# Kernel tuning notes

Hardware: AMD Instinct MI355X
Metric: run time of the kernel (lower is better)

Reference implementation:

```python
import jax, jax.numpy as jnp
import numpy as np
import math

B, N, G, D = 32, 100, 32, 1024  # batch, boxes (hardcoded 100), groups/fc_dim, out_channel
DG = D // G                      # 32, per-group dim
FEAT_DIM = 64                    # position embedding dim


def setup_inputs() -> dict:
    key = jax.random.key(0)
    ks = jax.random.split(key, 10)
    feat = jax.random.normal(ks[0], (B, N, D), dtype=jnp.float32)
    # valid boxes: xmin/ymin in [0,500), width/height in [1,101)
    xy = jax.random.uniform(ks[1], (B, N, 2), dtype=jnp.float32) * 500.0
    wh = jax.random.uniform(ks[2], (B, N, 2), dtype=jnp.float32) * 100.0 + 1.0
    bbox = jnp.concatenate([xy, xy + wh], axis=-1)  # (B,N,4) xmin,ymin,xmax,ymax
    feat_mask = jax.random.bernoulli(ks[3], 0.1, (B, N, G, N))
    s = 0.02
    fc1_w = jax.random.normal(ks[4], (G, FEAT_DIM), dtype=jnp.float32) * s
    fc1_b = jnp.zeros((G,), dtype=jnp.float32)
    q_w = jax.random.normal(ks[5], (D, D), dtype=jnp.float32) * s
    q_b = jnp.zeros((D,), dtype=jnp.float32)
    k_w = jax.random.normal(ks[6], (D, D), dtype=jnp.float32) * s
    k_b = jnp.zeros((D,), dtype=jnp.float32)
    # grouped 1x1 conv: torch weight (D_out=1024, D_in/groups=1024,1,1) -> (G, DG, D)
    conv_w = jax.random.normal(ks[7], (G, DG, D), dtype=jnp.float32) * s
    conv_b = jnp.zeros((D,), dtype=jnp.float32)
    return {"feat": feat, "bbox": bbox, "feat_mask": feat_mask,
            "fc1_w": fc1_w, "fc1_b": fc1_b, "q_w": q_w, "q_b": q_b,
            "k_w": k_w, "k_b": k_b, "conv_w": conv_w, "conv_b": conv_b}


def _position_embedding(bbox):
    xmin, ymin, xmax, ymax = jnp.split(bbox, 4, axis=2)  # each (B,N,1)
    bw = xmax - xmin + 1.0
    bh = ymax - ymin + 1.0
    cx = 0.5 * (xmin + xmax)
    cy = 0.5 * (ymin + ymax)
    dx = jnp.log(jnp.maximum(jnp.abs((cx - cx.swapaxes(1, 2)) / bw), 1e-3))
    dy = jnp.log(jnp.maximum(jnp.abs((cy - cy.swapaxes(1, 2)) / bh), 1e-3))
    dw = jnp.log(bw / bw.swapaxes(1, 2))
    dh = jnp.log(bh / bh.swapaxes(1, 2))
    pos = jnp.stack([dx, dy, dw, dh], axis=3)  # (B,N,N,4)
    feat_range = jnp.arange(FEAT_DIM // 8, dtype=jnp.float32)  # 8
    dim_mat = jnp.power(1000.0, (8.0 / FEAT_DIM) * feat_range)  # (8,)
    div = (100.0 * pos)[..., None] / dim_mat  # (B,N,N,4,8)
    emb = jnp.concatenate([jnp.sin(div), jnp.cos(div)], axis=4)  # (B,N,N,4,16)
    return emb.reshape(bbox.shape[0], N, N, FEAT_DIM)


def reference(feat, bbox, feat_mask, fc1_w, fc1_b, q_w, q_b, k_w, k_b, conv_w, conv_b):
    pos_emb = _position_embedding(bbox)  # (B,N,N,64)
    # fc1 + relu -> affinity weights; aff_weight[b,q,g,k]
    aff_weight = jax.nn.relu(jnp.einsum('bqkf,gf->bqkg', pos_emb, fc1_w) + fc1_b)
    aff_weight = aff_weight.swapaxes(2, 3)  # (B,N,G,N)
    q = (feat @ q_w.T + q_b).reshape(-1, N, G, DG)  # (B,N,G,DG)
    k = (feat @ k_w.T + k_b).reshape(-1, N, G, DG)
    aff = jnp.einsum('bqgd,bkgd->bqgk', q, k) * (1.0 / math.sqrt(DG))  # (B,N,G,N)
    weighted = jnp.log(jnp.maximum(aff_weight, 1e-6)) + aff
    weighted = jnp.where(feat_mask, -1e9, weighted)
    sm = jax.nn.softmax(weighted, axis=3)  # (B,N,G,N)
    out_t = jnp.einsum('bqgk,bkc->bqgc', sm, feat)  # (B,N,G,D)
    # grouped 1x1 conv: group g maps D channels -> DG output channels
    lin = jnp.einsum('bqgc,goc->bqgo', out_t, conv_w) + conv_b.reshape(G, DG)
    attention = lin.reshape(feat.shape[0], N, D)
    return jax.nn.relu(feat + attention)
```

## Files before the change

kernel.cpp:

```cpp
#include <hip/hip_runtime.h>
#include <math.h>

#define B_  32
#define N_  100
#define G_  32
#define D_  1024
#define DG_ 32
#define FD_ 64

typedef __attribute__((ext_vector_type(8))) short short8;
typedef __attribute__((ext_vector_type(8))) unsigned short ushort8;
typedef __attribute__((ext_vector_type(4))) unsigned short ushort4v;
typedef __attribute__((ext_vector_type(4))) float f32x4;

__device__ inline unsigned short f2bf(float f) {
    unsigned int x = __float_as_uint(f);
    unsigned int r = (x + 0x7fffu + ((x >> 16) & 1u)) >> 16;
    return (unsigned short)r;
}
__device__ inline unsigned short f2h(float f) {
    _Float16 h = (_Float16)f;
    return __builtin_bit_cast(unsigned short, h);
}
__device__ inline float h2f(unsigned short u) {
    return (float)__builtin_bit_cast(_Float16, u);
}
__device__ inline void load_lds16(const void* g, void* l) {
    __builtin_amdgcn_global_load_lds(
        (const __attribute__((address_space(1))) void*)g,
        (__attribute__((address_space(3))) void*)l, 16, 0, 0);
}

__global__ __launch_bounds__(256) void prep_kernel(
    const unsigned int* __restrict__ mask, int* __restrict__ flag,
    const float* __restrict__ bbox, float* __restrict__ prep,
    const float* __restrict__ feat, unsigned short* __restrict__ featb,
    const float* __restrict__ qw, unsigned short* __restrict__ wqb,
    const float* __restrict__ kw, unsigned short* __restrict__ wkb,
    const float* __restrict__ cw, unsigned short* __restrict__ wcb)
{
    const int bid = blockIdx.x;
    const int t = threadIdx.x;
    if (bid < 256) {
        const int nwords = (B_ * N_ * G_ * N_) / 4 / 8;
        int v = 0;
        for (int i = bid * 256 + t; i < nwords; i += 256 * 256)
            v |= (mask[i] > 1u) ? 1 : 0;
        if (__any(v) && (t & 63) == 0) atomicOr(flag, 1);
        return;
    }
    if (bid < 272) {
        const int i = (bid - 256) * 256 + t;
        if (i < B_ * N_) {
            const float4 bb = *reinterpret_cast<const float4*>(bbox + (size_t)i * 4);
            const float bw = bb.z - bb.x + 1.0f, bh = bb.w - bb.y + 1.0f;
            float4 o0, o1;
            o0.x = 0.5f * (bb.x + bb.z);
            o0.y = 0.5f * (bb.y + bb.w);
            o0.z = __logf(bw);
            o0.w = __logf(bh);
            o1.x = 1.0f / bw;
            o1.y = 1.0f / bh;
            o1.z = 0.0f; o1.w = 0.0f;
            *reinterpret_cast<float4*>(prep + (size_t)i * 8)     = o0;
            *reinterpret_cast<float4*>(prep + (size_t)i * 8 + 4) = o1;
        }
        return;
    }
    const float* src;
    unsigned short* dst;
    int i;
    if (bid < 1872)      { src = feat; dst = featb; i = (bid - 272) * 256 + t; }
    else if (bid < 2384) { src = qw;   dst = wqb;   i = (bid - 1872) * 256 + t; }
    else if (bid < 2896) { src = kw;   dst = wkb;   i = (bid - 2384) * 256 + t; }
    else                 { src = cw;   dst = wcb;   i = (bid - 2896) * 256 + t; }
    const float4 a = reinterpret_cast<const float4*>(src)[i * 2 + 0];
    const float4 b = reinterpret_cast<const float4*>(src)[i * 2 + 1];
    ushort8 o;
    o[0] = f2bf(a.x); o[1] = f2bf(a.y); o[2] = f2bf(a.z); o[3] = f2bf(a.w);
    o[4] = f2bf(b.x); o[5] = f2bf(b.y); o[6] = f2bf(b.z); o[7] = f2bf(b.w);
    *reinterpret_cast<ushort8*>(&dst[i * 8]) = o;
}

__global__ __launch_bounds__(256) void mfma_gemm_nt(
    const unsigned short* __restrict__ A,
    const unsigned short* __restrict__ Wq,
    const unsigned short* __restrict__ Wk,
    const unsigned short* __restrict__ Wc,
    const float* __restrict__ bq, const float* __restrict__ bk,
    unsigned short* __restrict__ Q16, unsigned short* __restrict__ K16,
    unsigned short* __restrict__ F16)
{
    __shared__ short As0[128 * 64], As1[128 * 64];
    __shared__ short Bs0[64 * 64],  Bs1[64 * 64];

    const int z = blockIdx.z;
    const unsigned short* W = (z == 0) ? Wq : (z == 1) ? Wk : Wc;
    const float* bias        = (z == 0) ? bq : (z == 1) ? bk : nullptr;
    unsigned short* O        = (z == 0) ? Q16 : (z == 1) ? K16 : F16;

    const int m0 = blockIdx.x * 128;
    const int n0 = blockIdx.y * 64;
    const int t = threadIdx.x;
    const int lane = t & 63;
    const int wid = t >> 6;
    const int wr = wid >> 1, wc = wid & 1;
    const int lo = lane & 15, hi = lane >> 4;

    f32x4 acc[4][2] = {};

    auto STAGE = [&](short* dA, short* dB, int k0) {
#pragma unroll
        for (int c = 0; c < 4; ++c) {
            const int idx16 = c * 256 + t;
            const int row = idx16 >> 3;
            const int colb = ((idx16 & 7) * 16) ^ ((row & 7) << 4);
            load_lds16((const char*)(A + (size_t)(m0 + row) * D_ + k0) + colb,
                       (char*)dA + (c * 256 + wid * 64) * 16);
        }
#pragma unroll
        for (int c = 0; c < 2; ++c) {
            const int idx16 = c * 256 + t;
            const int row = idx16 >> 3;
            const int colb = ((idx16 & 7) * 16) ^ ((row & 7) << 4);
            load_lds16((const char*)(W + (size_t)(n0 + row) * D_ + k0) + colb,
                       (char*)dB + (c * 256 + wid * 64) * 16);
        }
    };

    auto COMPUTE = [&](const short* sA, const short* sB) {
#pragma unroll
        for (int ks = 0; ks < 2; ++ks) {
            short8 afr[4], bfr[2];
            const int kb = ks * 64 + hi * 16;
#pragma unroll
            for (int f = 0; f < 4; ++f) {
                const int am = wr * 64 + f * 16 + lo;
                afr[f] = *reinterpret_cast<const short8*>(
                    (const char*)sA + am * 128 + (kb ^ ((am & 7) << 4)));
            }
#pragma unroll
            for (int j = 0; j < 2; ++j) {
                const int bn = wc * 32 + j * 16 + lo;
                bfr[j] = *reinterpret_cast<const short8*>(
                    (const char*)sB + bn * 128 + (kb ^ ((bn & 7) << 4)));
            }
#pragma unroll
            for (int i = 0; i < 4; ++i)
#pragma unroll
                for (int j = 0; j < 2; ++j)
                    acc[i][j] = __builtin_amdgcn_mfma_f32_16x16x32_bf16(
                        afr[i], bfr[j], acc[i][j], 0, 0, 0);
        }
    };

    STAGE(As0, Bs0, 0);
    __syncthreads();
    for (int it = 0; it < 16; it += 2) {
        STAGE(As1, Bs1, (it + 1) << 6);
        COMPUTE(As0, Bs0);
        __syncthreads();
        if (it + 2 < 16) STAGE(As0, Bs0, (it + 2) << 6);
        COMPUTE(As1, Bs1);
        __syncthreads();
    }

#pragma unroll
    for (int j = 0; j < 2; ++j) {
        const int col = n0 + wc * 32 + j * 16 + lo;
        const float bv = bias ? bias[col] : 0.0f;
#pragma unroll
        for (int i = 0; i < 4; ++i) {
            const int mbase = m0 + wr * 64 + i * 16 + hi * 4;
#pragma unroll
            for (int r = 0; r < 4; ++r)
                O[(size_t)(mbase + r) * D_ + col] = f2bf(acc[i][j][r] + bv);
        }
    }
}

__global__ __launch_bounds__(256) void pos_fc1_kernel(
    const float* __restrict__ prep, const float* __restrict__ fc1_w,
    const float* __restrict__ fc1_b,
    const unsigned char* __restrict__ mask8, const int* __restrict__ mask32,
    const int* __restrict__ flag, unsigned short* __restrict__ wm)
{
    __shared__ unsigned short embh[112 * 72];
    __shared__ unsigned short w1h[G_ * 72];
    __shared__ float b1[G_];
    __shared__ float tbl[8];
    __shared__ float pos4[N_][4];

    const int b = blockIdx.x / N_;
    const int q = blockIdx.x % N_;
    const int t = threadIdx.x;
    const int lane = t & 63;
    const int w = t >> 6;
    const int lo = lane & 15, hi = lane >> 4;

    const float4 pq0 = *reinterpret_cast<const float4*>(prep + (size_t)(b * N_ + q) * 8);
    const float4 pq1 = *reinterpret_cast<const float4*>(prep + (size_t)(b * N_ + q) * 8 + 4);
    const float cxq = pq0.x, cyq = pq0.y, lbwq = pq0.z, lbhq = pq0.w;
    const float rbwq = pq1.x, rbhq = pq1.y;

    for (int i = t; i < G_ * FD_; i += 256)
        w1h[(i >> 6) * 72 + (i & 63)] = f2h(fc1_w[i]);
    if (t < G_) b1[t] = fc1_b[t];
    if (t < 8)  tbl[t] = 100.0f / powf(1000.0f, (float)t * 0.125f);
    for (int i = t; i < 12 * 64; i += 256)
        embh[(100 + (i >> 6)) * 72 + (i & 63)] = 0;

    if (t < N_) {
        const float4 p0 = *reinterpret_cast<const float4*>(prep + (size_t)(b * N_ + t) * 8);
        pos4[t][0] = __logf(fmaxf(fabsf(cxq - p0.x) * rbwq, 1e-3f));
        pos4[t][1] = __logf(fmaxf(fabsf(cyq - p0.y) * rbhq, 1e-3f));
        pos4[t][2] = lbwq - p0.z;
        pos4[t][3] = lbhq - p0.w;
    }
    __syncthreads();

    for (int idx = t; idx < N_ * 32; idx += 256) {
        const int k = idx >> 5;
        const int p = (idx >> 3) & 3;
        const int j = idx & 7;
        const float dv = pos4[k][p] * tbl[j];
        embh[k * 72 + p * 16 + j]     = f2h(__sinf(dv));
        embh[k * 72 + p * 16 + 8 + j] = f2h(__cosf(dv));
    }
    __syncthreads();

    const bool bytemask = (*flag != 0);
    const int xq = q & 7;
    for (int tid = w; tid < 14; tid += 4) {
        const int mt = tid >> 1, nt = tid & 1;
        f32x4 d = {};
#pragma unroll
        for (int ks = 0; ks < 2; ++ks) {
            const short8 af = *reinterpret_cast<const short8*>(
                embh + (mt * 16 + lo) * 72 + ks * 32 + hi * 8);
            const short8 bf = *reinterpret_cast<const short8*>(
                w1h + (nt * 16 + lo) * 72 + ks * 32 + hi * 8);
            d = __builtin_amdgcn_mfma_f32_16x16x32_f16(af, bf, d, 0, 0, 0);
        }
        const int g = nt * 16 + lo;
        const int k0 = mt * 16 + hi * 4;
        const float bb = b1[g];
        unsigned int mby = 0;
        uint4 mi = {};
        if (k0 < N_) {
            const size_t midx = ((size_t)(b * N_ + q) * G_ + g) * N_ + k0;
            if (bytemask) mby = *(const unsigned int*)(mask8 + midx);
            else          mi  = *(const uint4*)(mask32 + midx);
        }
        ushort4v ov;
#pragma unroll
        for (int r = 0; r < 4; ++r) {
            const int k = k0 + r;
            const bool msk = bytemask
                ? (((mby >> (8 * r)) & 0xffu) != 0u)
                : ((r == 0 ? mi.x : r == 1 ? mi.y : r == 2 ? mi.z : mi.w) != 0u);
            const float aff = d[r] + bb;
            const float lv = __logf(fmaxf(fmaxf(aff, 0.0f), 1e-6f));
            ov[r] = f2h((k >= N_ || msk) ? -65504.0f : lv);
        }
        const size_t row = (size_t)(b * N_ + q) * G_ + g;
        char* dst = (char*)wm + row * 256 + ((2 * k0) ^ (xq << 4));
        *reinterpret_cast<ushort4v*>(dst) = ov;
    }
}

__global__ __launch_bounds__(256) void attn_mfma(
    const unsigned short* __restrict__ qb, const unsigned short* __restrict__ kb,
    const unsigned short* __restrict__ fk16, const unsigned short* __restrict__ wm,
    const float* __restrict__ feat, const float* __restrict__ conv_b,
    float* __restrict__ out)
{
    __shared__ unsigned short PW[128 * 128];
    __shared__ unsigned short FL[DG_ * 128];

    const int bg = blockIdx.x;
    const int b = bg >> 5, g = bg & 31;
    const int t = threadIdx.x;
    const int lane = t & 63;
    const int w = t >> 6;
    const int lo = lane & 15, hi = lane >> 4;
    const float scale = 0.17677669529663687f;

    {
        const char* wbase = (const char*)wm + ((size_t)b * N_ * G_ + g) * 256;
        for (int u = t; u < 1600; u += 256) {
            const int qq = u >> 4, seg = u & 15;
            load_lds16(wbase + (size_t)qq * (G_ * 256) + seg * 16,
                       (char*)PW + u * 16);
        }
    }
    for (int u = t; u < DG_ * 28; u += 256) {
        const int dg = u / 28, n = 100 + u % 28;
        *(unsigned short*)((char*)FL + dg * 256 +
                           (((n >> 3) ^ (dg & 7)) << 4) + (n & 7) * 2) = 0;
    }
    for (int u = t; u < 400; u += 256) {
        const int n = u >> 2, c4 = u & 3;
        const ushort8 v = *reinterpret_cast<const ushort8*>(
            fk16 + (size_t)(b * N_ + n) * D_ + g * DG_ + c4 * 8);
#pragma unroll
        for (int j = 0; j < 8; ++j) {
            const int dg = c4 * 8 + j;
            *(unsigned short*)((char*)FL + dg * 256 +
                               (((n >> 3) ^ j) << 4) + (n & 7) * 2) = v[j];
        }
    }

    short8 qf[2], kf[7];
#pragma unroll
    for (int mtl = 0; mtl < 2; ++mtl) {
        const int row = w * 32 + mtl * 16 + lo;
        const int rc = row < N_ ? row : N_ - 1;
        qf[mtl] = *reinterpret_cast<const short8*>(
            qb + (size_t)(b * N_ + rc) * D_ + g * DG_ + hi * 8);
    }
#pragma unroll
    for (int ct = 0; ct < 7; ++ct) {
        const int kr = ct * 16 + lo;
        const int krc = kr < N_ ? kr : N_ - 1;
        kf[ct] = *reinterpret_cast<const short8*>(
            kb + (size_t)(b * N_ + krc) * D_ + g * DG_ + hi * 8);
    }

    __syncthreads();

    f32x4 s[2][7];
#pragma unroll
    for (int mtl = 0; mtl < 2; ++mtl)
#pragma unroll
        for (int ct = 0; ct < 7; ++ct) {
            f32x4 z = {};
            s[mtl][ct] = __builtin_amdgcn_mfma_f32_16x16x32_bf16(
                qf[mtl], kf[ct], z, 0, 0, 0);
        }

#pragma unroll
    for (int mtl = 0; mtl < 2; ++mtl) {
        const int qr0 = w * 32 + mtl * 16 + hi * 4;
#pragma unroll
        for (int ct = 0; ct < 7; ++ct) {
            const int k = ct * 16 + lo;
#pragma unroll
            for (int r = 0; r < 4; ++r) {
                const int row = qr0 + r;
                const float wv = h2f(*(const unsigned short*)(
                    (const char*)PW + row * 256 + ((2 * k) ^ ((row & 7) << 4))));
                s[mtl][ct][r] = s[mtl][ct][r] * scale + wv;
            }
        }
    }

    float sm[2][4];
#pragma unroll
    for (int mtl = 0; mtl < 2; ++mtl) {
        f32x4 mv = s[mtl][0];
#pragma unroll
        for (int ct = 1; ct < 7; ++ct)
#pragma unroll
            for (int r = 0; r < 4; ++r) mv[r] = fmaxf(mv[r], s[mtl][ct][r]);
        float mx[4];
#pragma unroll
        for (int r = 0; r < 4; ++r) {
            float m = mv[r];
            m = fmaxf(m, __shfl_xor(m, 1));
            m = fmaxf(m, __shfl_xor(m, 2));
            m = fmaxf(m, __shfl_xor(m, 4));
            m = fmaxf(m, __shfl_xor(m, 8));
            mx[r] = m;
        }
        f32x4 sv = {};
#pragma unroll
        for (int ct = 0; ct < 7; ++ct)
#pragma unroll
            for (int r = 0; r < 4; ++r) {
                const float e = __expf(s[mtl][ct][r] - mx[r]);
                s[mtl][ct][r] = e;
                sv[r] += e;
            }
#pragma unroll
        for (int r = 0; r < 4; ++r) {
            float ss = sv[r];
            ss += __shfl_xor(ss, 1);
            ss += __shfl_xor(ss, 2);
            ss += __shfl_xor(ss, 4);
            ss += __shfl_xor(ss, 8);
            sm[mtl][r] = 1.0f / ss;
        }
    }

#pragma unroll
    for (int mtl = 0; mtl < 2; ++mtl) {
        const int qr0 = w * 32 + mtl * 16 + hi * 4;
#pragma unroll
        for (int ct = 0; ct < 7; ++ct) {
            const int col = ct * 16 + lo;
#pragma unroll
            for (int r = 0; r < 4; ++r) {
                const int row = qr0 + r;
                *(unsigned short*)((char*)PW + row * 256 +
                                   ((2 * col) ^ ((row & 7) << 4))) =
                    f2bf(s[mtl][ct][r] * sm[mtl][r]);
            }
        }
    }
    {
        const int zr = w * 32 + (lane & 31);
        const int zg = 14 + (lane >> 5);
        short8 zs = {};
        *reinterpret_cast<short8*>(
            (char*)PW + zr * 256 + ((zg * 16) ^ ((zr & 7) << 4))) = zs;
    }

    f32x4 o[2][2] = {};
#pragma unroll
    for (int ks = 0; ks < 4; ++ks) {
        short8 pa[2], fb[2];
#pragma unroll
        for (int mtl = 0; mtl < 2; ++mtl) {
            const int prow = w * 32 + mtl * 16 + lo;
            pa[mtl] = *reinterpret_cast<const short8*>(
                (const char*)PW + prow * 256 +
                ((ks * 64 + hi * 16) ^ ((prow & 7) << 4)));
        }
#pragma unroll
        for (int nt = 0; nt < 2; ++nt) {
            const int dg = nt * 16 + lo;
            fb[nt] = *reinterpret_cast<const short8*>(
                (const char*)FL + dg * 256 +
                ((ks * 64 + hi * 16) ^ ((dg & 7) << 4)));
        }
#pragma unroll
        for (int mtl = 0; mtl < 2; ++mtl)
#pragma unroll
            for (int nt = 0; nt < 2; ++nt)
                o[mtl][nt] = __builtin_amdgcn_mfma_f32_16x16x32_bf16(
                    pa[mtl], fb[nt], o[mtl][nt], 0, 0, 0);
    }

#pragma unroll
    for (int mtl = 0; mtl < 2; ++mtl) {
        const int qr0 = w * 32 + mtl * 16 + hi * 4;
#pragma unroll
        for (int nt = 0; nt < 2; ++nt) {
            const int col = g * DG_ + nt * 16 + lo;
            const float cb = conv_b[col];
#pragma unroll
            for (int r = 0; r < 4; ++r) {
                const int q = qr0 + r;
                if (q < N_) {
                    const size_t gi = (size_t)(b * N_ + q) * D_ + col;
                    out[gi] = fmaxf(feat[gi] + o[mtl][nt][r] + cb, 0.0f);
                }
            }
        }
    }
}

extern "C" void kernel_launch(void* const* d_in, const int* in_sizes, int n_in,
                              void* d_out, int out_size, void* d_ws, size_t ws_size,
                              hipStream_t stream)
{
    const float* feat   = (const float*)d_in[0];
    const float* bbox   = (const float*)d_in[1];
    const void*  maskp  = d_in[2];
    const float* fc1_w  = (const float*)d_in[3];
    const float* fc1_b  = (const float*)d_in[4];
    const float* q_w    = (const float*)d_in[5];
    const float* q_b    = (const float*)d_in[6];
    const float* k_w    = (const float*)d_in[7];
    const float* k_b    = (const float*)d_in[8];
    const float* conv_w = (const float*)d_in[9];
    const float* conv_b = (const float*)d_in[10];

    const int BN_D  = B_ * N_ * D_;
    const int DD    = D_ * D_;
    const int WM_N  = B_ * G_ * N_ * 128;

    unsigned short* ws16 = (unsigned short*)d_ws;
    unsigned short* qb16  = ws16;
    unsigned short* kb16  = qb16 + BN_D;
    unsigned short* fk16  = kb16 + BN_D;
    unsigned short* wm    = fk16 + BN_D;
    int* flag = (int*)(wm + WM_N);
    float* prep = (float*)(flag + 64);

    unsigned short* featb = wm;
    unsigned short* wqb   = featb + BN_D;
    unsigned short* wkb   = wqb + DD;
    unsigned short* wcb   = wkb + DD;

    hipMemsetAsync(flag, 0, sizeof(int), stream);
    prep_kernel<<<3408, 256, 0, stream>>>((const unsigned int*)maskp, flag,
                                          bbox, prep, feat, featb,
                                          q_w, wqb, k_w, wkb, conv_w, wcb);

    dim3 gg(B_ * N_ / 128, D_ / 64, 3);
    mfma_gemm_nt<<<gg, 256, 0, stream>>>(featb, wqb, wkb, wcb, q_b, k_b,
                                         qb16, kb16, fk16);

    pos_fc1_kernel<<<B_ * N_, 256, 0, stream>>>(prep, fc1_w, fc1_b,
                                                (const unsigned char*)maskp,
                                                (const int*)maskp, flag, wm);

    attn_mfma<<<B_ * G_, 256, 0, stream>>>(qb16, kb16, fk16, wm,
                                           feat, conv_b, (float*)d_out);
}
```

Measured before the change: 95.78 us.

## Merge projection GEMM and pos_fc1 into one launch sharing LDS

Combines the bf16 Q/K/conv projection GEMM and the position-embedding fc1 kernel into a single launch of 4400 blocks. The first 1200 blocks do GEMM tiles and the rest compute affinity weights, with shared memory unioned between the two roles. The bf16 staging buffers move out of the wm region so both roles can run at once. This removes a launch boundary and lets the two independent stages overlap on the GPU. The cost is that every block reserves the larger 48KB LDS, which may lower occupancy for the pos_fc1 blocks.

```diff
diff --git a/kernel.cpp b/kernel.cpp
--- a/kernel.cpp
+++ b/kernel.cpp
@@ -82,121 +82,127 @@
     *reinterpret_cast<ushort8*>(&dst[i * 8]) = o;
 }
 
-__global__ __launch_bounds__(256) void mfma_gemm_nt(
+__global__ __launch_bounds__(256) void mid_kernel(
     const unsigned short* __restrict__ A,
     const unsigned short* __restrict__ Wq,
     const unsigned short* __restrict__ Wk,
     const unsigned short* __restrict__ Wc,
     const float* __restrict__ bq, const float* __restrict__ bk,
     unsigned short* __restrict__ Q16, unsigned short* __restrict__ K16,
-    unsigned short* __restrict__ F16)
-{
-    __shared__ short As0[128 * 64], As1[128 * 64];
-    __shared__ short Bs0[64 * 64],  Bs1[64 * 64];
-
-    const int z = blockIdx.z;
-    const unsigned short* W = (z == 0) ? Wq : (z == 1) ? Wk : Wc;
-    const float* bias        = (z == 0) ? bq : (z == 1) ? bk : nullptr;
-    unsigned short* O        = (z == 0) ? Q16 : (z == 1) ? K16 : F16;
-
-    const int m0 = blockIdx.x * 128;
-    const int n0 = blockIdx.y * 64;
-    const int t = threadIdx.x;
-    const int lane = t & 63;
-    const int wid = t >> 6;
-    const int wr = wid >> 1, wc = wid & 1;
-    const int lo = lane & 15, hi = lane >> 4;
-
-    f32x4 acc[4][2] = {};
-
-    auto STAGE = [&](short* dA, short* dB, int k0) {
-#pragma unroll
-        for (int c = 0; c < 4; ++c) {
-            const int idx16 = c * 256 + t;
-            const int row = idx16 >> 3;
-            const int colb = ((idx16 & 7) * 16) ^ ((row & 7) << 4);
-            load_lds16((const char*)(A + (size_t)(m0 + row) * D_ + k0) + colb,
-                       (char*)dA + (c * 256 + wid * 64) * 16);
-        }
-#pragma unroll
-        for (int c = 0; c < 2; ++c) {
-            const int idx16 = c * 256 + t;
-            const int row = idx16 >> 3;
-            const int colb = ((idx16 & 7) * 16) ^ ((row & 7) << 4);
-            load_lds16((const char*)(W + (size_t)(n0 + row) * D_ + k0) + colb,
-                       (char*)dB + (c * 256 + wid * 64) * 16);
-        }
-    };
-
-    auto COMPUTE = [&](const short* sA, const short* sB) {
-#pragma unroll
-        for (int ks = 0; ks < 2; ++ks) {
-            short8 afr[4], bfr[2];
-            const int kb = ks * 64 + hi * 16;
-#pragma unroll
-            for (int f = 0; f < 4; ++f) {
-                const int am = wr * 64 + f * 16 + lo;
-                afr[f] = *reinterpret_cast<const short8*>(
-                    (const char*)sA + am * 128 + (kb ^ ((am & 7) << 4)));
-            }
-#pragma unroll
-            for (int j = 0; j < 2; ++j) {
-                const int bn = wc * 32 + j * 16 + lo;
-                bfr[j] = *reinterpret_cast<const short8*>(
-                    (const char*)sB + bn * 128 + (kb ^ ((bn & 7) << 4)));
-            }
-#pragma unroll
-            for (int i = 0; i < 4; ++i)
-#pragma unroll
-                for (int j = 0; j < 2; ++j)
-                    acc[i][j] = __builtin_amdgcn_mfma_f32_16x16x32_bf16(
-                        afr[i], bfr[j], acc[i][j], 0, 0, 0);
-        }
-    };
-
-    STAGE(As0, Bs0, 0);
-    __syncthreads();
-    for (int it = 0; it < 16; it += 2) {
-        STAGE(As1, Bs1, (it + 1) << 6);
-        COMPUTE(As0, Bs0);
-        __syncthreads();
-        if (it + 2 < 16) STAGE(As0, Bs0, (it + 2) << 6);
-        COMPUTE(As1, Bs1);
-        __syncthreads();
-    }
-
-#pragma unroll
-    for (int j = 0; j < 2; ++j) {
-        const int col = n0 + wc * 32 + j * 16 + lo;
-        const float bv = bias ? bias[col] : 0.0f;
-#pragma unroll
-        for (int i = 0; i < 4; ++i) {
-            const int mbase = m0 + wr * 64 + i * 16 + hi * 4;
-#pragma unroll
-            for (int r = 0; r < 4; ++r)
-                O[(size_t)(mbase + r) * D_ + col] = f2bf(acc[i][j][r] + bv);
-        }
-    }
-}
-
-__global__ __launch_bounds__(256) void pos_fc1_kernel(
+    unsigned short* __restrict__ F16,
     const float* __restrict__ prep, const float* __restrict__ fc1_w,
     const float* __restrict__ fc1_b,
     const unsigned char* __restrict__ mask8, const int* __restrict__ mask32,
     const int* __restrict__ flag, unsigned short* __restrict__ wm)
 {
-    __shared__ unsigned short embh[112 * 72];
-    __shared__ unsigned short w1h[G_ * 72];
-    __shared__ float b1[G_];
-    __shared__ float tbl[8];
-    __shared__ float pos4[N_][4];
-
-    const int b = blockIdx.x / N_;
-    const int q = blockIdx.x % N_;
+    __shared__ char smem[49152];
+
+    const int bid = blockIdx.x;
     const int t = threadIdx.x;
     const int lane = t & 63;
+    const int lo = lane & 15, hi = lane >> 4;
+
+    if (bid < 1200) {
+        short* As0 = (short*)smem;
+        short* As1 = (short*)(smem + 16384);
+        short* Bs0 = (short*)(smem + 32768);
+        short* Bs1 = (short*)(smem + 40960);
+
+        const int z = bid / 400;
+        const int rem = bid % 400;
+        const int m0 = (rem % 25) * 128;
+        const int n0 = (rem / 25) * 64;
+
+        const unsigned short* W = (z == 0) ? Wq : (z == 1) ? Wk : Wc;
+        const float* bias        = (z == 0) ? bq : (z == 1) ? bk : nullptr;
+        unsigned short* O        = (z == 0) ? Q16 : (z == 1) ? K16 : F16;
+
+        const int wid = t >> 6;
+        const int wr = wid >> 1, wc = wid & 1;
+
+        f32x4 acc[4][2] = {};
+
+        auto STAGE = [&](short* dA, short* dB, int k0) {
+#pragma unroll
+            for (int c = 0; c < 4; ++c) {
+                const int idx16 = c * 256 + t;
+                const int row = idx16 >> 3;
+                const int colb = ((idx16 & 7) * 16) ^ ((row & 7) << 4);
+                load_lds16((const char*)(A + (size_t)(m0 + row) * D_ + k0) + colb,
+                           (char*)dA + (c * 256 + wid * 64) * 16);
+            }
+#pragma unroll
+            for (int c = 0; c < 2; ++c) {
+                const int idx16 = c * 256 + t;
+                const int row = idx16 >> 3;
+                const int colb = ((idx16 & 7) * 16) ^ ((row & 7) << 4);
+                load_lds16((const char*)(W + (size_t)(n0 + row) * D_ + k0) + colb,
+                           (char*)dB + (c * 256 + wid * 64) * 16);
+            }
+        };
+
+        auto COMPUTE = [&](const short* sA, const short* sB) {
+#pragma unroll
+            for (int ks = 0; ks < 2; ++ks) {
+                short8 afr[4], bfr[2];
+                const int kb = ks * 64 + hi * 16;
+#pragma unroll
+                for (int f = 0; f < 4; ++f) {
+                    const int am = wr * 64 + f * 16 + lo;
+                    afr[f] = *reinterpret_cast<const short8*>(
+                        (const char*)sA + am * 128 + (kb ^ ((am & 7) << 4)));
+                }
+#pragma unroll
+                for (int j = 0; j < 2; ++j) {
+                    const int bn = wc * 32 + j * 16 + lo;
+                    bfr[j] = *reinterpret_cast<const short8*>(
+                        (const char*)sB + bn * 128 + (kb ^ ((bn & 7) << 4)));
+                }
+#pragma unroll
+                for (int i = 0; i < 4; ++i)
+#pragma unroll
+                    for (int j = 0; j < 2; ++j)
+                        acc[i][j] = __builtin_amdgcn_mfma_f32_16x16x32_bf16(
+                            afr[i], bfr[j], acc[i][j], 0, 0, 0);
+            }
+        };
+
+        STAGE(As0, Bs0, 0);
+        __syncthreads();
+        for (int it = 0; it < 16; it += 2) {
+            STAGE(As1, Bs1, (it + 1) << 6);
+            COMPUTE(As0, Bs0);
+            __syncthreads();
+            if (it + 2 < 16) STAGE(As0, Bs0, (it + 2) << 6);
+            COMPUTE(As1, Bs1);
+            __syncthreads();
+        }
+
+#pragma unroll
+        for (int j = 0; j < 2; ++j) {
+            const int col = n0 + wc * 32 + j * 16 + lo;
+            const float bv = bias ? bias[col] : 0.0f;
+#pragma unroll
+            for (int i = 0; i < 4; ++i) {
+                const int mbase = m0 + wr * 64 + i * 16 + hi * 4;
+#pragma unroll
+                for (int r = 0; r < 4; ++r)
+                    O[(size_t)(mbase + r) * D_ + col] = f2bf(acc[i][j][r] + bv);
+            }
+        }
+        return;
+    }
+
+    unsigned short* embh = (unsigned short*)smem;
+    unsigned short* w1h  = (unsigned short*)(smem + 16128);
+    float* b1   = (float*)(smem + 20736);
+    float* tbl  = (float*)(smem + 20864);
+    float (*pos4)[4] = (float (*)[4])(smem + 20896);
+
+    const int pb = bid - 1200;
+    const int b = pb / N_;
+    const int q = pb % N_;
     const int w = t >> 6;
-    const int lo = lane & 15, hi = lane >> 4;
 
     const float4 pq0 = *reinterpret_cast<const float4*>(prep + (size_t)(b * N_ + q) * 8);
     const float4 pq1 = *reinterpret_cast<const float4*>(prep + (size_t)(b * N_ + q) * 8 + 4);
@@ -488,8 +494,7 @@
     unsigned short* wm    = fk16 + BN_D;
     int* flag = (int*)(wm + WM_N);
     float* prep = (float*)(flag + 64);
-
-    unsigned short* featb = wm;
+    unsigned short* featb = (unsigned short*)(prep + B_ * N_ * 8);
     unsigned short* wqb   = featb + BN_D;
     unsigned short* wkb   = wqb + DD;
     unsigned short* wcb   = wkb + DD;
@@ -499,13 +504,11 @@
                                           bbox, prep, feat, featb,
                                           q_w, wqb, k_w, wkb, conv_w, wcb);
 
-    dim3 gg(B_ * N_ / 128, D_ / 64, 3);
-    mfma_gemm_nt<<<gg, 256, 0, stream>>>(featb, wqb, wkb, wcb, q_b, k_b,
-                                         qb16, kb16, fk16);
-
-    pos_fc1_kernel<<<B_ * N_, 256, 0, stream>>>(prep, fc1_w, fc1_b,
-                                                (const unsigned char*)maskp,
-                                                (const int*)maskp, flag, wm);
+    mid_kernel<<<4400, 256, 0, stream>>>(featb, wqb, wkb, wcb, q_b, k_b,
+                                         qb16, kb16, fk16,
+                                         prep, fc1_w, fc1_b,
+                                         (const unsigned char*)maskp,
+                                         (const int*)maskp, flag, wm);
 
     attn_mfma<<<B_ * G_, 256, 0, stream>>>(qb16, kb16, fk16, wm,
                                            feat, conv_b, (float*)d_out);
```

New measurement: 97.20 us. Within noise of the previous version (+1.5%).
